# Optimization experiments

Measured on AMD Instinct MI355X. Metric: run time of the kernel, lower is better.

Reference implementation:

```python
import jax, jax.numpy as jnp
import numpy as np

# ---- constants mirroring the torch module ----
LOSS_ALPHA = 1.0      # args.loss_weight_alpha (intra-class weight)
LOSS_BETA = 1.0       # args.loss_weight_beta (focal weight)
FOCAL_GAMMA = 2.0
FOCAL_ALPHA = 0.85
EPS = 1e-09
LDAM_S = 30.0
CLS_NUM = np.array([85.0, 900.0])
LDAM_MAX_M = 0.5
LDAM_W = np.array([0.15, 0.85], dtype=np.float32)
B = 16777216


def setup_inputs() -> dict:
    key = jax.random.key(0)
    k1, k2 = jax.random.split(key)
    x = jax.random.uniform(k1, (B, 2), dtype=jnp.float32)  # [B, 2] probabilities-like logits
    target = jax.random.randint(k2, (B,), 0, 2)            # binary labels
    return {"x": x, "target": target}


def _intraclass_p(centered, std, target, cls):
    # correlation between consecutive same-class rows (sorted-index order),
    # vectorized: class-c indices first via stable argsort, mask invalid pairs.
    n_rows = centered.shape[0]
    mask = target == cls
    n = jnp.sum(mask)
    order = jnp.argsort(jnp.where(mask, jnp.arange(n_rows), n_rows))
    a, b = order[:-1], order[1:]
    corr = jnp.sum(centered[a] * centered[b], axis=1) / (std[a] * std[b])
    valid = jnp.arange(n_rows - 1) < (n - 1)
    s = jnp.sum(jnp.where(valid, corr, 0.0))
    return jnp.where(n > 0, s / jnp.maximum(n, 1).astype(s.dtype), 0.0)


def reference(x, target):
    num_cls = x.shape[1]
    # ---- LDAM loss ----
    m = 1.0 / np.sqrt(np.sqrt(CLS_NUM))
    m = m * (LDAM_MAX_M / np.max(m))
    m_list = jnp.asarray(m, jnp.float32)
    w = jnp.asarray(LDAM_W)
    batch_m = m_list[target]                                      # [B]
    onehot = jax.nn.one_hot(target, num_cls, dtype=bool)          # [B, C]
    out = jnp.where(onehot, x - batch_m[:, None], x)              # margin on target logit only
    logsm = jax.nn.log_softmax(LDAM_S * out, axis=-1)
    nll = -jnp.take_along_axis(logsm, target[:, None], axis=1)[:, 0]
    wi = w[target]
    ldam = jnp.sum(wi * nll) / jnp.sum(wi)                        # weighted-mean cross entropy
    # ---- binary focal loss (treats x[:,1] as probability) ----
    p = x[:, 1]
    t = target.astype(x.dtype)
    fl = (-FOCAL_ALPHA * t * (1.0 - p) ** FOCAL_GAMMA * jnp.log(p + EPS)
          - (1.0 - FOCAL_ALPHA) * (1.0 - t) * p ** FOCAL_GAMMA * jnp.log(1.0 - p + EPS))
    focal = jnp.mean(fl)
    # ---- intra-class correlation loss ----
    centered = x - jnp.mean(x, axis=1, keepdims=True)
    std = jnp.std(x, axis=1, ddof=1)                               # torch.std default: unbiased
    p0 = _intraclass_p(centered, std, target, 0)
    p1 = _intraclass_p(centered, std, target, 1)
    intra = (p0 - p1) ** 2
    return ldam + LOSS_BETA * focal + LOSS_ALPHA * intra
```

## Files before the change

kernel.cpp:

```cpp
#include <hip/hip_runtime.h>

#define E_BLOCK 8192
#define E_WAVE  2048
#define QITERS  8

#define M1f     0.2771814156f
#define C_A1    60.0f
#define C_C1    (30.0f*M1f - 15.0f)

#define EXP2F(v) __builtin_amdgcn_exp2f(v)
#define LOG2F(v) __builtin_amdgcn_logf(v)

struct BlockRec {
  int s0, p0, s1, p1;
  float wnll, fl;
  int cnt1, pad;
};

__device__ __forceinline__ void comb0(int &s, int &f, int &l, int sb, int fb, int lb) {
  s += sb + l * fb;
  f = f ? f : fb;
  l = fb ? lb : l;
}

__device__ __forceinline__ void bfly_step(int m, int lane, int &s, int &f, int &l) {
  const int os = __shfl_xor(s, m), of = __shfl_xor(f, m), ol = __shfl_xor(l, m);
  const bool up = (lane & m) != 0;
  int as = up ? os : s, af = up ? of : f, al = up ? ol : l;
  const int bs = up ? s : os, bf = up ? f : of, bl = up ? l : ol;
  comb0(as, af, al, bs, bf, bl);
  s = as; f = af; l = al;
}

__device__ __forceinline__ void elem_math(float x0, float x1, int t, int k,
                                          float &wnll, float &flraw, int &cnt1,
                                          unsigned int &word) {
  const float tf  = (float)t;
  const float wgt = fmaf(tf, 0.7f, 0.15f);
  const float d   = x0 - x1;
  const float za  = fmaf(tf, C_A1, -30.0f);
  const float zc  = fmaf(tf, C_C1, 15.0f);
  const float z   = fmaf(za, d, zc);
  const float ex  = EXP2F(fabsf(z) * -1.44269504f);
  const float lp  = LOG2F(1.0f + ex);
  const float sp  = fmaf(0.69314718f, lp, fmaxf(z, 0.0f));
  wnll = fmaf(wgt, sp, wnll);
  const float om  = 1.0f - x1;
  const float q   = t ? x1 : om;
  const float r   = t ? om : x1;
  const float lg2 = LOG2F(q + 1e-9f);
  const float wr2 = (wgt * r) * r;
  flraw = fmaf(wr2, lg2, flraw);
  cnt1 += t;
  const unsigned int code = 4u | (unsigned int)(d > 0.0f) | ((unsigned int)t << 1);
  word |= code << (8 * k);
}

__global__ __launch_bounds__(256, 8) void loss_pass1(
    const float* __restrict__ x, const int* __restrict__ tgt,
    BlockRec* __restrict__ recs, int B) {
  __shared__ unsigned int lds[3328];
  unsigned int* chunkw = lds;
  unsigned int* stw = lds + 2304;
  float* wnw = (float*)(lds + 2560);
  float* flw = (float*)(lds + 2816);
  int*   cnw = (int*)(lds + 3072);

  const int tid = threadIdx.x;
  const int w = tid >> 6, lane = tid & 63;
  const int waveBase = blockIdx.x * E_BLOCK + w * E_WAVE;

  float wnll = 0.f, flraw = 0.f; int cnt1 = 0;

  if (waveBase + E_WAVE <= B) {
    const int e0 = waveBase + lane * 4;
    const float4* __restrict__ px = (const float4*)(x + 2 * (size_t)e0);
    const int4*   __restrict__ pt = (const int4*)(tgt + e0);

    float4 xa = px[0], xb = px[1];
    int4  t4 = pt[0];
    for (int j = 0; j < QITERS; ++j) {
      float4 xa_n, xb_n; int4 t4_n;
      if (j + 1 < QITERS) {
        const int o = (j + 1) * 128;
        xa_n = px[o]; xb_n = px[o + 1]; t4_n = pt[(j + 1) * 64];
      }
      unsigned int word = 0;
      elem_math(xa.x, xa.y, t4.x, 0, wnll, flraw, cnt1, word);
      elem_math(xa.z, xa.w, t4.y, 1, wnll, flraw, cnt1, word);
      elem_math(xb.x, xb.y, t4.z, 2, wnll, flraw, cnt1, word);
      elem_math(xb.z, xb.w, t4.w, 3, wnll, flraw, cnt1, word);
      const int qi = w * 512 + (j << 6) + lane;
      chunkw[(qi >> 3) * 9 + (qi & 7)] = word;
      xa = xa_n; xb = xb_n; t4 = t4_n;
    }
  } else {
    for (int j = 0; j < QITERS; ++j) {
      unsigned int word = 0;
      for (int k = 0; k < 4; ++k) {
        const int e = waveBase + ((j << 6) + lane) * 4 + k;
        if (e < B) {
          elem_math(x[2 * (size_t)e], x[2 * (size_t)e + 1], tgt[e], k,
                    wnll, flraw, cnt1, word);
        }
      }
      const int qi = w * 512 + (j << 6) + lane;
      chunkw[(qi >> 3) * 9 + (qi & 7)] = word;
    }
  }
  __syncthreads();

  int s0 = 0, f0 = 0, l0 = 0, s1 = 0, f1 = 0, l1 = 0;
  #pragma unroll
  for (int r = 0; r < 8; ++r) {
    const unsigned int wv = chunkw[tid * 9 + r];
    #pragma unroll
    for (int k = 0; k < 4; ++k) {
      const unsigned int b = (wv >> (8 * k)) & 7u;
      if (b & 4u) {
        const int sv = (int)((b & 1u) << 1) - 1;
        const int t  = (int)((b >> 1) & 1u);
        const int lv = t ? l1 : l0;
        const int add = lv * sv;
        if (t) { s1 += add; l1 = sv; f1 = f1 ? f1 : sv; }
        else   { s0 += add; l0 = sv; f0 = f0 ? f0 : sv; }
      }
    }
  }
  stw[tid] = (unsigned)(s0 + 128) | ((unsigned)(f0 + 1) << 8) | ((unsigned)(l0 + 1) << 10)
           | ((unsigned)(s1 + 128) << 16) | ((unsigned)(f1 + 1) << 24) | ((unsigned)(l1 + 1) << 26);
  wnw[tid] = wnll; flw[tid] = flraw * -0.69314718f; cnw[tid] = cnt1;
  __syncthreads();

  if (w == 0) {
    int S0 = 0, F0 = 0, L0 = 0, S1 = 0, F1 = 0, L1 = 0;
    float W = 0.f, F = 0.f; int C = 0;
    #pragma unroll
    for (int q = 0; q < 4; ++q) {
      const int i = lane * 4 + q;
      const unsigned int pk = stw[i];
      comb0(S0, F0, L0, (int)(pk & 255u) - 128, (int)((pk >> 8) & 3u) - 1, (int)((pk >> 10) & 3u) - 1);
      comb0(S1, F1, L1, (int)((pk >> 16) & 255u) - 128, (int)((pk >> 24) & 3u) - 1, (int)((pk >> 26) & 3u) - 1);
      W += wnw[i]; F += flw[i]; C += cnw[i];
    }
    #pragma unroll
    for (int k = 0; k < 6; ++k) {
      const int m = 1 << k;
      bfly_step(m, lane, S0, F0, L0);
      bfly_step(m, lane, S1, F1, L1);
      W += __shfl_xor(W, m); F += __shfl_xor(F, m); C += __shfl_xor(C, m);
    }
    if (lane == 0) {
      BlockRec r;
      r.s0 = S0; r.p0 = (F0 + 1) | ((L0 + 1) << 4);
      r.s1 = S1; r.p1 = (F1 + 1) | ((L1 + 1) << 4);
      r.wnll = W; r.fl = F; r.cnt1 = C; r.pad = 0;
      recs[blockIdx.x] = r;
    }
  }
}

__global__ __launch_bounds__(256) void loss_pass2(
    const BlockRec* __restrict__ recs, int NB, int B, float* __restrict__ out) {
  __shared__ int sS0[256], sF0[256], sL0[256], sS1[256], sF1[256], sL1[256], sC[256];
  __shared__ double sW[256], sFl[256];
  const int tid = threadIdx.x, w = tid >> 6, lane = tid & 63;
  const int R = (NB + 255) >> 8;

  int s0 = 0, f0 = 0, l0 = 0, s1 = 0, f1 = 0, l1 = 0;
  double W = 0.0, Fd = 0.0; int C = 0;
  for (int r = 0; r < R; ++r) {
    const int b = tid * R + r;
    if (b < NB) {
      const BlockRec rec = recs[b];
      comb0(s0, f0, l0, rec.s0, (rec.p0 & 3) - 1, ((rec.p0 >> 4) & 3) - 1);
      comb0(s1, f1, l1, rec.s1, (rec.p1 & 3) - 1, ((rec.p1 >> 4) & 3) - 1);
      W += (double)rec.wnll; Fd += (double)rec.fl; C += rec.cnt1;
    }
  }
  sS0[tid] = s0; sF0[tid] = f0; sL0[tid] = l0;
  sS1[tid] = s1; sF1[tid] = f1; sL1[tid] = l1;
  sC[tid] = C; sW[tid] = W; sFl[tid] = Fd;
  __syncthreads();

  if (w == 0) {
    int S0 = 0, F0 = 0, L0 = 0, S1 = 0, F1 = 0, L1 = 0; int Ct = 0;
    double Wt = 0.0, Ft = 0.0;
    #pragma unroll
    for (int q = 0; q < 4; ++q) {
      const int i = lane * 4 + q;
      comb0(S0, F0, L0, sS0[i], sF0[i], sL0[i]);
      comb0(S1, F1, L1, sS1[i], sF1[i], sL1[i]);
      Wt += sW[i]; Ft += sFl[i]; Ct += sC[i];
    }
    #pragma unroll
    for (int k = 0; k < 6; ++k) {
      const int m = 1 << k;
      bfly_step(m, lane, S0, F0, L0);
      bfly_step(m, lane, S1, F1, L1);
      Wt += __shfl_xor(Wt, m); Ft += __shfl_xor(Ft, m); Ct += __shfl_xor(Ct, m);
    }
    if (lane == 0) {
      const double n1 = (double)Ct, n0 = (double)B - n1;
      const double sw = 0.15 * n0 + 0.85 * n1;
      const double ldam  = Wt / sw;
      const double focal = Ft / (double)B;
      const double q0 = (n0 > 0.0) ? (double)S0 / n0 : 0.0;
      const double q1 = (n1 > 0.0) ? (double)S1 / n1 : 0.0;
      const double dq = q0 - q1;
      out[0] = (float)(ldam + focal + dq * dq);
    }
  }
}

extern "C" void kernel_launch(void* const* d_in, const int* in_sizes, int n_in,
                              void* d_out, int out_size, void* d_ws, size_t ws_size,
                              hipStream_t stream) {
  const float* x  = (const float*)d_in[0];
  const int* tgt  = (const int*)d_in[1];
  float* out      = (float*)d_out;
  const int B  = in_sizes[1];
  const int NB = (B + E_BLOCK - 1) / E_BLOCK;
  BlockRec* recs = (BlockRec*)d_ws;
  loss_pass1<<<NB, 256, 0, stream>>>(x, tgt, recs, B);
  loss_pass2<<<1, 256, 0, stream>>>(recs, NB, B, out);
}
```

Before: 247.2 us.

## Stage pass1 loads through LDS with async global_load_lds double buffering

Replaces the register-prefetched float4 loads in pass1 with asynchronous global-to-LDS loads, double-buffered per wave over four sub-chunks, with explicit vmcnt waits. The launch bound drops to 2 blocks per CU because LDS use grows to about 61KB per block. The intent is to keep more memory traffic in flight per wave and hide HBM latency, at the cost of lower occupancy and extra LDS round trips. Correctness relies on global_load_lds lane-to-address mapping and on the hand-written waitcnt encoding.

New measurement: 240.7 us. -2.6%, faster.

```diff
diff --git a/kernel.cpp b/kernel.cpp
--- a/kernel.cpp
+++ b/kernel.cpp
@@ -2,6 +2,8 @@
 
 #define E_BLOCK 8192
 #define E_WAVE  2048
+#define SUB     512
+#define NSUB    4
 #define QITERS  8
 
 #define M1f     0.2771814156f
@@ -10,6 +12,8 @@
 
 #define EXP2F(v) __builtin_amdgcn_exp2f(v)
 #define LOG2F(v) __builtin_amdgcn_logf(v)
+
+#define VMCNT_IMM(N) (((N)&15) | (((N)>>4)<<14) | (7<<4) | (15<<8))
 
 struct BlockRec {
   int s0, p0, s1, p1;
@@ -56,15 +60,26 @@
   word |= code << (8 * k);
 }
 
-__global__ __launch_bounds__(256, 8) void loss_pass1(
+__device__ __forceinline__ void load_lds16f(const float* g, unsigned int* l) {
+  __builtin_amdgcn_global_load_lds(
+      (const __attribute__((address_space(1))) void*)g,
+      (__attribute__((address_space(3))) void*)l, 16, 0, 0);
+}
+__device__ __forceinline__ void load_lds16i(const int* g, unsigned int* l) {
+  __builtin_amdgcn_global_load_lds(
+      (const __attribute__((address_space(1))) void*)g,
+      (__attribute__((address_space(3))) void*)l, 16, 0, 0);
+}
+
+__global__ __launch_bounds__(256, 2) void loss_pass1(
     const float* __restrict__ x, const int* __restrict__ tgt,
     BlockRec* __restrict__ recs, int B) {
-  __shared__ unsigned int lds[3328];
-  unsigned int* chunkw = lds;
-  unsigned int* stw = lds + 2304;
-  float* wnw = (float*)(lds + 2560);
-  float* flw = (float*)(lds + 2816);
-  int*   cnw = (int*)(lds + 3072);
+  __shared__ unsigned int lds[15616];
+  unsigned int* chunkw = lds + 12288;
+  unsigned int* stw = lds + 14592;
+  float* wnw = (float*)(lds + 14848);
+  float* flw = (float*)(lds + 15104);
+  int*   cnw = (int*)(lds + 15360);
 
   const int tid = threadIdx.x;
   const int w = tid >> 6, lane = tid & 63;
@@ -73,26 +88,44 @@
   float wnll = 0.f, flraw = 0.f; int cnt1 = 0;
 
   if (waveBase + E_WAVE <= B) {
-    const int e0 = waveBase + lane * 4;
-    const float4* __restrict__ px = (const float4*)(x + 2 * (size_t)e0);
-    const int4*   __restrict__ pt = (const int4*)(tgt + e0);
-
-    float4 xa = px[0], xb = px[1];
-    int4  t4 = pt[0];
-    for (int j = 0; j < QITERS; ++j) {
-      float4 xa_n, xb_n; int4 t4_n;
-      if (j + 1 < QITERS) {
-        const int o = (j + 1) * 128;
-        xa_n = px[o]; xb_n = px[o + 1]; t4_n = pt[(j + 1) * 64];
+    unsigned int* const wbase = lds + w * 3072;
+
+    auto issue = [&](int s, int bsel) {
+      const int sb = waveBase + s * SUB;
+      unsigned int* lbx = wbase + bsel * 1536;
+      unsigned int* lbt = lbx + 1024;
+      #pragma unroll
+      for (int i = 0; i < 4; ++i)
+        load_lds16f(x + 2 * (size_t)sb + i * 256 + lane * 4, lbx + i * 256);
+      #pragma unroll
+      for (int i = 0; i < 2; ++i)
+        load_lds16i(tgt + sb + i * 256 + lane * 4, lbt + i * 256);
+    };
+
+    issue(0, 0);
+    issue(1, 1);
+
+    #pragma unroll
+    for (int s = 0; s < NSUB; ++s) {
+      if (s < NSUB - 1) __builtin_amdgcn_s_waitcnt(VMCNT_IMM(6));
+      else              __builtin_amdgcn_s_waitcnt(VMCNT_IMM(0));
+      const char* lbx = (const char*)(wbase + (s & 1) * 1536);
+      const char* lbt = lbx + 4096;
+      #pragma unroll
+      for (int h = 0; h < 2; ++h) {
+        const int qq = lane + h * 64;
+        const float4 xa = *(const float4*)(lbx + qq * 32);
+        const float4 xb = *(const float4*)(lbx + qq * 32 + 16);
+        const int4  t4 = *(const int4*)(lbt + qq * 16);
+        unsigned int word = 0;
+        elem_math(xa.x, xa.y, t4.x, 0, wnll, flraw, cnt1, word);
+        elem_math(xa.z, xa.w, t4.y, 1, wnll, flraw, cnt1, word);
+        elem_math(xb.x, xb.y, t4.z, 2, wnll, flraw, cnt1, word);
+        elem_math(xb.z, xb.w, t4.w, 3, wnll, flraw, cnt1, word);
+        const int qi = w * 512 + s * 128 + qq;
+        chunkw[(qi >> 3) * 9 + (qi & 7)] = word;
       }
-      unsigned int word = 0;
-      elem_math(xa.x, xa.y, t4.x, 0, wnll, flraw, cnt1, word);
-      elem_math(xa.z, xa.w, t4.y, 1, wnll, flraw, cnt1, word);
-      elem_math(xb.x, xb.y, t4.z, 2, wnll, flraw, cnt1, word);
-      elem_math(xb.z, xb.w, t4.w, 3, wnll, flraw, cnt1, word);
-      const int qi = w * 512 + (j << 6) + lane;
-      chunkw[(qi >> 3) * 9 + (qi & 7)] = word;
-      xa = xa_n; xb = xb_n; t4 = t4_n;
+      if (s + 2 < NSUB) issue(s + 2, s & 1);
     }
   } else {
     for (int j = 0; j < QITERS; ++j) {
```
